# Performance work log

Hardware: AMD Instinct MI355X
Metric: run time of the kernel (lower is better)

The kernel has to match this reference:

```python
import jax, jax.numpy as jnp
import numpy as np

EPS_BN = 1e-5
EPS_NORM = 1e-12


def setup_inputs() -> dict:
    dim, mid, k = 128, 32, 3
    b, h, w = 8, 128, 128
    key = jax.random.key(0)
    ks = jax.random.split(key, 16)
    s = 0.05
    return {
        "x": jax.random.normal(ks[0], (b, dim, h, w), jnp.float32),
        "w_spatial_in": jax.random.normal(ks[1], (dim, dim), jnp.float32) * s,
        "w_dw_spatial": jax.random.normal(ks[2], (dim, 1, k), jnp.float32) * s,
        "w_spatial_out": jax.random.normal(ks[3], (dim, dim), jnp.float32) * s,
        "w_ch_in": jax.random.normal(ks[4], (dim, dim), jnp.float32) * s,
        "w_ch_dw": jax.random.normal(ks[5], (dim, 1, k), jnp.float32) * s,
        "w_ch_out": jax.random.normal(ks[6], (dim, dim), jnp.float32) * s,
        "w_mlp1": jax.random.normal(ks[7], (mid, dim), jnp.float32) * s,
        "b_mlp1": jax.random.normal(ks[8], (mid,), jnp.float32) * s,
        "w_mlp2": jax.random.normal(ks[9], (dim, mid), jnp.float32) * s,
        "b_mlp2": jax.random.normal(ks[10], (dim,), jnp.float32) * s,
        "diff_weight": jnp.float32(1.0),
        "bn_gamma": jnp.ones((dim,), jnp.float32),
        "bn_beta": jnp.zeros((dim,), jnp.float32),
        "w_out_proj": jax.random.normal(ks[11], (dim, dim), jnp.float32) * s,
    }


def _dwconv1d(seq, wk):
    # seq: [b, c, L], wk: [c, 1, k] depthwise, 'same' padding
    c = seq.shape[1]
    k = wk.shape[-1]
    return jax.lax.conv_general_dilated(
        seq, wk, window_strides=(1,), padding=[(k // 2, k // 2)],
        dimension_numbers=("NCH", "OIH", "NCH"), feature_group_count=c)


def _ocs_forward(x, w_spatial_in, w_dw_spatial, w_spatial_out,
                 w_ch_in, w_ch_dw, w_ch_out,
                 w_mlp1, b_mlp1, w_mlp2, b_mlp2,
                 diff_weight, bn_gamma, bn_beta, w_out_proj):
    b, c, h, w = x.shape
    L = h * w
    alpha = beta = eta = 1.0

    # ---- scan indices (4 orders) ----
    idx_row = jnp.arange(L)
    gy, gx = jnp.meshgrid(jnp.arange(h), jnp.arange(w), indexing="ij")
    idx_col = (gx * h + gy).reshape(-1)
    orders = [idx_row, idx_row[::-1], idx_col, idx_col[::-1]]

    x_seq0 = x.reshape(b, c, L).transpose(0, 2, 1)  # [b, L, c]

    def scan(idx):
        s = x_seq0[:, idx]                                   # gather   [b,L,c]
        s = jnp.einsum("blc,oc->blo", s, w_spatial_in)       # linear
        s = _dwconv1d(s.transpose(0, 2, 1), w_dw_spatial)    # dw conv  [b,c,L]
        s = jnp.einsum("bcl,oc->blo", s, w_spatial_out)      # linear   [b,L,c]
        s = s.at[:, idx].set(s[:, jnp.arange(L)]) if False else s[:, jnp.argsort(idx)]  # scatter back (inverse perm)
        return s.transpose(0, 2, 1).reshape(b, c, h, w)

    y_sp = (scan(orders[0]) + scan(orders[1]) + scan(orders[2]) + scan(orders[3])) * 0.25

    # ---- channel branch ----
    seq = x.reshape(b, c, L)
    seq = jnp.einsum("oc,bcl->bol", w_ch_in, seq)
    seq = _dwconv1d(seq, w_ch_dw)
    seq = jnp.einsum("oc,bcl->bol", w_ch_out, seq)
    gap = x.mean((2, 3))                                     # [b,c]
    gap = gap / jnp.maximum(jnp.linalg.norm(gap, axis=1, keepdims=True), EPS_NORM)
    m = jnp.einsum("bi,bj->bij", gap, gap)                   # [b,c,c]
    seq_agg = jnp.einsum("bij,bjl->bil", m, seq)             # [b,c,L]
    h1 = jax.nn.silu(jnp.einsum("mc,bcl->bml", w_mlp1, seq_agg) + b_mlp1[None, :, None])
    y_ch = (jnp.einsum("cm,bml->bcl", w_mlp2, h1) + b_mlp2[None, :, None]).reshape(b, c, h, w)

    # ---- difference branch (reflect-pad 4-neighbor abs diff) ----
    p = jnp.pad(x, ((0, 0), (0, 0), (1, 1), (1, 1)), mode="reflect")
    cx = p[:, :, 1:-1, 1:-1]
    diff = (jnp.abs(cx - p[:, :, 1:-1, :-2]) + jnp.abs(cx - p[:, :, 1:-1, 2:])
            + jnp.abs(cx - p[:, :, :-2, 1:-1]) + jnp.abs(cx - p[:, :, 2:, 1:-1])) * 0.25
    y_diff = x + diff_weight * diff

    # ---- combine, 1x1 proj, batchnorm (training-mode batch stats) ----
    y = alpha * y_sp + beta * y_ch + eta * y_diff
    y = jnp.einsum("oc,bchw->bohw", w_out_proj, y)
    mu = y.mean((0, 2, 3))
    var = y.var((0, 2, 3))
    y = (y - mu[None, :, None, None]) * jax.lax.rsqrt(var + EPS_BN)[None, :, None, None]
    y = y * bn_gamma[None, :, None, None] + bn_beta[None, :, None, None]
    return y


def reference(x, w_spatial_in, w_dw_spatial, w_spatial_out, w_ch_in, w_ch_dw,
              w_ch_out, w_mlp1, b_mlp1, w_mlp2, b_mlp2, diff_weight,
              bn_gamma, bn_beta, w_out_proj):
    return _ocs_forward(x, w_spatial_in, w_dw_spatial, w_spatial_out,
                        w_ch_in, w_ch_dw, w_ch_out, w_mlp1, b_mlp1,
                        w_mlp2, b_mlp2, diff_weight, bn_gamma, bn_beta,
                        w_out_proj)
```

## Files before the change

kernel.cpp:

```cpp
#include <hip/hip_runtime.h>
#include <hip/hip_bf16.h>

#define C 128
#define L 16384
#define B 8
#define MID 32
#define NBL (B * L)

typedef unsigned short ushort_t;
typedef __attribute__((ext_vector_type(8))) short s8v;
typedef __attribute__((ext_vector_type(4))) float f4v;
typedef __attribute__((ext_vector_type(8))) float f8v;

__device__ __forceinline__ unsigned short f2bf(float f) {
    union { float f; unsigned int u; } a; a.f = f;
    unsigned int u = a.u;
    return (unsigned short)((u + 0x7fffu + ((u >> 16) & 1u)) >> 16);
}

__device__ __forceinline__ f8v unp8(s8v v) {
    f8v f;
#pragma unroll
    for (int j = 0; j < 8; j++) f[j] = __uint_as_float(((unsigned int)(unsigned short)v[j]) << 16);
    return f;
}

__device__ __forceinline__ f8v ldf8(const float* p) {
    float4 a = *(const float4*)p;
    float4 b = *(const float4*)(p + 4);
    f8v f;
    f[0] = a.x; f[1] = a.y; f[2] = a.z; f[3] = a.w;
    f[4] = b.x; f[5] = b.y; f[6] = b.z; f[7] = b.w;
    return f;
}

__device__ __forceinline__ int widx(int slot, int o, int w) {
    return ((slot * 8 + (o >> 4)) * 64 + (w >> 3) * 16 + (o & 15)) * 8 + (w & 7);
}

__global__ __launch_bounds__(256) void k_cvt(const float* __restrict__ x,
                                             ushort_t* __restrict__ xb,
                                             float* __restrict__ gap) {
    __shared__ float xs[64][129];
    const int bid = blockIdx.x;
    const int b = bid >> 8;
    const int l0 = (bid & 255) * 64;
    const int tid = threadIdx.x;
    const int c = tid >> 1, h = tid & 1;
    const float* src = x + ((size_t)(b * C + c)) * L + l0 + h * 32;
    float s = 0.f;
#pragma unroll
    for (int j = 0; j < 8; j++) {
        float4 v = *(const float4*)(src + j * 4);
        s += (v.x + v.y) + (v.z + v.w);
        int lb = h * 32 + j * 4;
        xs[lb + 0][c] = v.x; xs[lb + 1][c] = v.y;
        xs[lb + 2][c] = v.z; xs[lb + 3][c] = v.w;
    }
    s += __shfl_xor(s, 1);
    if (h == 0) atomicAdd(&gap[b * C + c], s);
    __syncthreads();
    const int l = tid & 63, quarter = tid >> 6, cb = quarter * 32;
    union { ushort_t hh[32]; uint4 q[4]; } u;
#pragma unroll
    for (int k = 0; k < 32; k++) u.hh[k] = f2bf(xs[l][cb + k]);
    uint4* dst = (uint4*)(xb + ((size_t)(b * L + l0 + l)) * C + cb);
#pragma unroll
    for (int k = 0; k < 4; k++) dst[k] = u.q[k];
}

__global__ __launch_bounds__(128) void k_prep_b(const float* __restrict__ gap,
                                                const float* __restrict__ w1,
                                                const float* __restrict__ Wco,
                                                const float* __restrict__ wcd,
                                                const float* __restrict__ Wci,
                                                float* __restrict__ a,
                                                float* __restrict__ pv) {
    int b = blockIdx.x, c = threadIdx.x;
    __shared__ float gl[C];
    __shared__ float red[C];
    __shared__ float gws[C];
    float v = gap[b * C + c] * (1.f / (float)L);
    red[c] = v * v;
    __syncthreads();
    for (int w = 64; w > 0; w >>= 1) {
        if (c < w) red[c] += red[c + w];
        __syncthreads();
    }
    float nrm = fmaxf(sqrtf(red[0]), 1e-12f);
    gl[c] = v / nrm;
    __syncthreads();
    if (c < MID) {
        float s = 0.f;
        for (int k = 0; k < C; k++) s = fmaf(w1[c * C + k], gl[k], s);
        a[b * MID + c] = s;
    }
    {
        float s = 0.f;
        for (int k = 0; k < C; k++) s = fmaf(gl[k], Wco[k * C + c], s);
        gws[c] = s;
    }
    __syncthreads();
    float p0 = 0.f, p1 = 0.f, p2 = 0.f;
    for (int cc = 0; cc < C; cc++) {
        float wv = Wci[cc * C + c];
        float g = gws[cc];
        p0 = fmaf(g * wcd[3 * cc], wv, p0);
        p1 = fmaf(g * wcd[3 * cc + 1], wv, p1);
        p2 = fmaf(g * wcd[3 * cc + 2], wv, p2);
    }
    pv[b * 384 + c] = p0;
    pv[b * 384 + 128 + c] = p1;
    pv[b * 384 + 256 + c] = p2;
}

__global__ __launch_bounds__(128) void k_prep_w(const float* __restrict__ Win,
                                                const float* __restrict__ Wproj,
                                                const float* __restrict__ Wout,
                                                const float* __restrict__ w2,
                                                const float* __restrict__ b2,
                                                const float* __restrict__ wds,
                                                ushort_t* __restrict__ Wf,
                                                float* __restrict__ bp) {
    int o = blockIdx.x, c = threadIdx.x;
    __shared__ float pr[C];
    __shared__ float wct[C];
    pr[c] = Wproj[o * C + c];
    __syncthreads();
    {
        float s = 0.f;
        for (int k = 0; k < C; k++) s = fmaf(pr[k], Wout[k * C + c], s);
        wct[c] = s;
    }
    __syncthreads();
    float a1 = 0.f, as = 0.f;
    for (int cc = 0; cc < C; cc++) {
        float w = wct[cc];
        float win = Win[cc * C + c];
        a1 = fmaf(w * wds[3 * cc + 1], win, a1);
        as = fmaf(w * (0.25f * (wds[3 * cc] + wds[3 * cc + 2])), win, as);
    }
    const int slot = c >> 5, wi = c & 31;
    Wf[widx(slot, o, wi)] = f2bf(a1);
    Wf[widx(4 + slot, o, wi)] = f2bf(as);
    Wf[widx(8 + slot, o, wi)] = f2bf(pr[c]);
    if (c < MID) {
        float s2 = 0.f;
        for (int k = 0; k < C; k++) s2 = fmaf(pr[k], w2[k * MID + c], s2);
        Wf[widx(12, o, c)] = f2bf(s2);
    }
    if (c == 0) {
        float s3 = 0.f;
        for (int k = 0; k < C; k++) s3 = fmaf(pr[k], b2[k], s3);
        bp[o] = s3;
    }
}

__global__ __launch_bounds__(1024) __attribute__((amdgpu_waves_per_eu(4, 4)))
void k_fused(const ushort_t* __restrict__ xb,
             const ushort_t* __restrict__ Wf,
             const float* __restrict__ pv,
             const float* __restrict__ a,
             const float* __restrict__ b1,
             const float* __restrict__ pdw,
             const float* __restrict__ bp,
             float* __restrict__ outp,
             float* __restrict__ stats) {
    __shared__ ushort_t wlf[53248];
    __shared__ float sdst[C];
    __shared__ float sdsq[C];
    const int tid = threadIdx.x;
    int bid = blockIdx.x;
    bid = (bid & 7) * 64 + (bid >> 3);
    const int b = bid >> 6;
    const int y0 = (bid & 63) << 1;

#pragma unroll
    for (int i = 0; i < 7; i++) {
        int idx = tid + i * 1024;
        if (idx < 6656) ((uint4*)wlf)[idx] = ((const uint4*)Wf)[idx];
    }
    if (tid < C) { sdst[tid] = 0.f; sdsq[tid] = 0.f; }

    const int wave = tid >> 6, lane = tid & 63;
    const int n = lane & 15, q = lane >> 4;
    const int y = y0 + (wave >> 3);
    const int xg = (wave & 7) * 16 + n;
    const int l = y * 128 + xg;
    const size_t rb = (size_t)b * L;

    const int rL = (l > 0) ? (l - 1) : -1;
    const int rR = (l < L - 1) ? (l + 1) : -1;
    const int rU = (y > 0) ? (l - 128) : ((xg > 0) ? (16256 + xg - 1) : -1);
    const int rD = (y < 127) ? (l + 128) : ((xg < 127) ? (xg + 1) : -1);
    const int rlc = (rL >= 0) ? rL : 0;
    const int rrc = (rR >= 0) ? rR : 0;
    const int ruc = (rU >= 0) ? rU : 0;
    const int rdc = (rD >= 0) ? rD : 0;

    const float dwt4 = pdw[0] * 0.25f;
    const ushort_t* xrow = xb + (rb + l) * C;

    f4v acc[8];
#pragma unroll
    for (int i = 0; i < 8; i++) acc[i] = (f4v){0.f, 0.f, 0.f, 0.f};
    float s1 = 0.f;

    __syncthreads();

#define AF(slot, mt) (*(const s8v*)(wlf + ((((slot) * 8 + (mt)) * 64 + lane) * 8)))

#pragma unroll
    for (int ks = 0; ks < 4; ks++) {
        const int c0 = ks * 32 + q * 8;
        s8v vc = *(const s8v*)(xrow + c0);
        s8v vl = *(const s8v*)(xb + (rb + rlc) * C + c0);
        s8v vr = *(const s8v*)(xb + (rb + rrc) * C + c0);
        s8v vu = *(const s8v*)(xb + (rb + ruc) * C + c0);
        s8v vd = *(const s8v*)(xb + (rb + rdc) * C + c0);
        if (rL < 0) vl = (s8v){0, 0, 0, 0, 0, 0, 0, 0};
        if (rR < 0) vr = (s8v){0, 0, 0, 0, 0, 0, 0, 0};
        if (rU < 0) vu = (s8v){0, 0, 0, 0, 0, 0, 0, 0};
        if (rD < 0) vd = (s8v){0, 0, 0, 0, 0, 0, 0, 0};

#pragma unroll
        for (int mt = 0; mt < 8; mt++)
            acc[mt] = __builtin_amdgcn_mfma_f32_16x16x32_bf16(AF(ks, mt), vc, acc[mt], 0, 0, 0);
#pragma unroll
        for (int mt = 0; mt < 8; mt++) {
            s8v af = AF(4 + ks, mt);
            acc[mt] = __builtin_amdgcn_mfma_f32_16x16x32_bf16(af, vl, acc[mt], 0, 0, 0);
            acc[mt] = __builtin_amdgcn_mfma_f32_16x16x32_bf16(af, vr, acc[mt], 0, 0, 0);
            acc[mt] = __builtin_amdgcn_mfma_f32_16x16x32_bf16(af, vu, acc[mt], 0, 0, 0);
            acc[mt] = __builtin_amdgcn_mfma_f32_16x16x32_bf16(af, vd, acc[mt], 0, 0, 0);
        }

        f8v xc = unp8(vc);
        f8v xl = unp8(vl);
        f8v xr = unp8(vr);
        {
            f8v p0 = ldf8(pv + b * 384 + c0);
            f8v p1 = ldf8(pv + b * 384 + 128 + c0);
            f8v p2 = ldf8(pv + b * 384 + 256 + c0);
#pragma unroll
            for (int j = 0; j < 8; j++) {
                s1 = fmaf(p1[j], xc[j], s1);
                s1 = fmaf(p0[j], xl[j], s1);
                s1 = fmaf(p2[j], xr[j], s1);
            }
        }

        f8v xu = unp8(vu);
        f8v xd = unp8(vd);
        f8v a1 = (xg > 0) ? xl : xr;
        f8v a2 = (xg < 127) ? xr : xl;
        f8v a3 = (y > 0) ? xu : xd;
        f8v a4 = (y < 127) ? xd : xu;
        s8v vy;
#pragma unroll
        for (int j = 0; j < 8; j++) {
            float d = fabsf(xc[j] - a1[j]) + fabsf(xc[j] - a2[j]) +
                      fabsf(xc[j] - a3[j]) + fabsf(xc[j] - a4[j]);
            vy[j] = (short)f2bf(fmaf(dwt4, d, xc[j]));
        }
#pragma unroll
        for (int mt = 0; mt < 8; mt++)
            acc[mt] = __builtin_amdgcn_mfma_f32_16x16x32_bf16(AF(8 + ks, mt), vy, acc[mt], 0, 0, 0);
    }

    s1 += __shfl_xor(s1, 16);
    s1 += __shfl_xor(s1, 32);
    {
        f8v av = ldf8(a + b * MID + q * 8);
        f8v bv = ldf8(b1 + q * 8);
        s8v fs;
#pragma unroll
        for (int j = 0; j < 8; j++) {
            float pre = fmaf(av[j], s1, bv[j]);
            fs[j] = (short)f2bf(pre / (1.f + __expf(-pre)));
        }
#pragma unroll
        for (int mt = 0; mt < 8; mt++)
            acc[mt] = __builtin_amdgcn_mfma_f32_16x16x32_bf16(AF(12, mt), fs, acc[mt], 0, 0, 0);
    }

#undef AF

#pragma unroll
    for (int mt = 0; mt < 8; mt++) {
        const int o0 = mt * 16 + q * 4;
        float4 bv4 = *(const float4*)(bp + o0);
#pragma unroll
        for (int i = 0; i < 4; i++) {
            float bai = (i == 0) ? bv4.x : (i == 1) ? bv4.y : (i == 2) ? bv4.z : bv4.w;
            float v = acc[mt][i] + bai;
            outp[((size_t)(b * C + o0 + i)) * L + l] = v;
            float s = v, sq = v * v;
            s += __shfl_xor(s, 1); sq += __shfl_xor(sq, 1);
            s += __shfl_xor(s, 2); sq += __shfl_xor(sq, 2);
            s += __shfl_xor(s, 4); sq += __shfl_xor(sq, 4);
            s += __shfl_xor(s, 8); sq += __shfl_xor(sq, 8);
            if (n == 0) {
                atomicAdd(&sdst[o0 + i], s);
                atomicAdd(&sdsq[o0 + i], sq);
            }
        }
    }
    __syncthreads();
    if (tid < C) {
        atomicAdd(&stats[tid], sdst[tid]);
        atomicAdd(&stats[C + tid], sdsq[tid]);
    }
}

__global__ void k_bnfin(const float* __restrict__ stats, const float* __restrict__ gamma,
                        const float* __restrict__ beta, float* __restrict__ scsh) {
    int o = threadIdx.x;
    float n = (float)NBL;
    float mu = stats[o] / n;
    float var = stats[C + o] / n - mu * mu;
    float sc = gamma[o] * rsqrtf(var + 1e-5f);
    scsh[o] = sc;
    scsh[C + o] = fmaf(-mu, sc, beta[o]);
}

__global__ __launch_bounds__(256) void k_bnapply(float* __restrict__ outp,
                                                 const float* __restrict__ scsh) {
    int bo = blockIdx.x;
    int o = bo & (C - 1);
    float sc = scsh[o], sh = scsh[C + o];
    float4* p = (float4*)(outp + (size_t)bo * L);
    for (int i = threadIdx.x; i < L / 4; i += 256) {
        float4 v = p[i];
        v.x = fmaf(v.x, sc, sh);
        v.y = fmaf(v.y, sc, sh);
        v.z = fmaf(v.z, sc, sh);
        v.w = fmaf(v.w, sc, sh);
        p[i] = v;
    }
}

extern "C" void kernel_launch(void* const* d_in, const int* in_sizes, int n_in,
                              void* d_out, int out_size, void* d_ws, size_t ws_size,
                              hipStream_t stream) {
    const float* x = (const float*)d_in[0];
    const float* Win = (const float*)d_in[1];
    const float* wds = (const float*)d_in[2];
    const float* Wout = (const float*)d_in[3];
    const float* Wci = (const float*)d_in[4];
    const float* wcd = (const float*)d_in[5];
    const float* Wco = (const float*)d_in[6];
    const float* w1 = (const float*)d_in[7];
    const float* b1 = (const float*)d_in[8];
    const float* w2 = (const float*)d_in[9];
    const float* b2 = (const float*)d_in[10];
    const float* pdw = (const float*)d_in[11];
    const float* gamma = (const float*)d_in[12];
    const float* beta = (const float*)d_in[13];
    const float* Wproj = (const float*)d_in[14];

    char* wsb = (char*)d_ws;
    ushort_t* xb = (ushort_t*)wsb;
    ushort_t* Wf = (ushort_t*)(wsb + 33554432);
    char* S = wsb + 176160768;
    float* gap  = (float*)(S + 0);
    float* stats= (float*)(S + 4096);
    float* scsh = (float*)(S + 5120);
    float* a    = (float*)(S + 6144);
    float* bp   = (float*)(S + 8192);
    float* pv   = (float*)(S + 12288);
    float* outp = (float*)d_out;

    hipMemsetAsync(S, 0, 5120, stream);
    k_cvt<<<2048, 256, 0, stream>>>(x, xb, gap);
    k_prep_b<<<8, 128, 0, stream>>>(gap, w1, Wco, wcd, Wci, a, pv);
    k_prep_w<<<128, 128, 0, stream>>>(Win, Wproj, Wout, w2, b2, wds, Wf, bp);
    k_fused<<<512, 1024, 0, stream>>>(xb, Wf, pv, a, b1, pdw, bp, outp, stats);
    k_bnfin<<<1, 128, 0, stream>>>(stats, gamma, beta, scsh);
    k_bnapply<<<1024, 256, 0, stream>>>(outp, scsh);
}
```

Before: 291.7 us.

## Merge prep kernels, fold BN finalize into apply, loop fused kernel over rows

Merges the two weight/batch prep kernels into one launch and folds the BN finalize step into the apply kernel, removing two kernel launches. The fused kernel now runs 256 blocks that each loop over two row pairs, so the 104KB weight tile is staged into LDS half as often. The per-batch pv vector is also cached in shared memory, and the channel-MLP term is computed before the main MFMA loop. Fewer blocks means less parallelism and a longer serial loop per block.

```diff
diff --git a/kernel.cpp b/kernel.cpp
--- a/kernel.cpp
+++ b/kernel.cpp
@@ -69,90 +69,93 @@
     for (int k = 0; k < 4; k++) dst[k] = u.q[k];
 }
 
-__global__ __launch_bounds__(128) void k_prep_b(const float* __restrict__ gap,
-                                                const float* __restrict__ w1,
-                                                const float* __restrict__ Wco,
-                                                const float* __restrict__ wcd,
-                                                const float* __restrict__ Wci,
-                                                float* __restrict__ a,
-                                                float* __restrict__ pv) {
-    int b = blockIdx.x, c = threadIdx.x;
-    __shared__ float gl[C];
-    __shared__ float red[C];
-    __shared__ float gws[C];
-    float v = gap[b * C + c] * (1.f / (float)L);
-    red[c] = v * v;
-    __syncthreads();
-    for (int w = 64; w > 0; w >>= 1) {
-        if (c < w) red[c] += red[c + w];
+__global__ __launch_bounds__(128) void k_prep(const float* __restrict__ Win,
+                                              const float* __restrict__ Wproj,
+                                              const float* __restrict__ Wout,
+                                              const float* __restrict__ w2,
+                                              const float* __restrict__ b2,
+                                              const float* __restrict__ wds,
+                                              const float* __restrict__ gap,
+                                              const float* __restrict__ w1,
+                                              const float* __restrict__ Wco,
+                                              const float* __restrict__ wcd,
+                                              const float* __restrict__ Wci,
+                                              ushort_t* __restrict__ Wf,
+                                              float* __restrict__ bp,
+                                              float* __restrict__ a,
+                                              float* __restrict__ pv) {
+    const int bid = blockIdx.x;
+    const int c = threadIdx.x;
+    if (bid < 128) {
+        const int o = bid;
+        __shared__ float pr[C];
+        __shared__ float wct[C];
+        pr[c] = Wproj[o * C + c];
         __syncthreads();
-    }
-    float nrm = fmaxf(sqrtf(red[0]), 1e-12f);
-    gl[c] = v / nrm;
-    __syncthreads();
-    if (c < MID) {
-        float s = 0.f;
-        for (int k = 0; k < C; k++) s = fmaf(w1[c * C + k], gl[k], s);
-        a[b * MID + c] = s;
-    }
-    {
-        float s = 0.f;
-        for (int k = 0; k < C; k++) s = fmaf(gl[k], Wco[k * C + c], s);
-        gws[c] = s;
-    }
-    __syncthreads();
-    float p0 = 0.f, p1 = 0.f, p2 = 0.f;
-    for (int cc = 0; cc < C; cc++) {
-        float wv = Wci[cc * C + c];
-        float g = gws[cc];
-        p0 = fmaf(g * wcd[3 * cc], wv, p0);
-        p1 = fmaf(g * wcd[3 * cc + 1], wv, p1);
-        p2 = fmaf(g * wcd[3 * cc + 2], wv, p2);
-    }
-    pv[b * 384 + c] = p0;
-    pv[b * 384 + 128 + c] = p1;
-    pv[b * 384 + 256 + c] = p2;
-}
-
-__global__ __launch_bounds__(128) void k_prep_w(const float* __restrict__ Win,
-                                                const float* __restrict__ Wproj,
-                                                const float* __restrict__ Wout,
-                                                const float* __restrict__ w2,
-                                                const float* __restrict__ b2,
-                                                const float* __restrict__ wds,
-                                                ushort_t* __restrict__ Wf,
-                                                float* __restrict__ bp) {
-    int o = blockIdx.x, c = threadIdx.x;
-    __shared__ float pr[C];
-    __shared__ float wct[C];
-    pr[c] = Wproj[o * C + c];
-    __syncthreads();
-    {
-        float s = 0.f;
-        for (int k = 0; k < C; k++) s = fmaf(pr[k], Wout[k * C + c], s);
-        wct[c] = s;
-    }
-    __syncthreads();
-    float a1 = 0.f, as = 0.f;
-    for (int cc = 0; cc < C; cc++) {
-        float w = wct[cc];
-        float win = Win[cc * C + c];
-        a1 = fmaf(w * wds[3 * cc + 1], win, a1);
-        as = fmaf(w * (0.25f * (wds[3 * cc] + wds[3 * cc + 2])), win, as);
-    }
-    const int slot = c >> 5, wi = c & 31;
-    Wf[widx(slot, o, wi)] = f2bf(a1);
-    Wf[widx(4 + slot, o, wi)] = f2bf(as);
-    Wf[widx(8 + slot, o, wi)] = f2bf(pr[c]);
-    if (c < MID) {
-        float s2 = 0.f;
-        for (int k = 0; k < C; k++) s2 = fmaf(pr[k], w2[k * MID + c], s2);
-        Wf[widx(12, o, c)] = f2bf(s2);
-    }
-    if (c == 0) {
-        float s3 = 0.f;
-        for (int k = 0; k < C; k++) s3 = fmaf(pr[k], b2[k], s3);
-        bp[o] = s3;
+        {
+            float s = 0.f;
+            for (int k = 0; k < C; k++) s = fmaf(pr[k], Wout[k * C + c], s);
+            wct[c] = s;
+        }
+        __syncthreads();
+        float a1 = 0.f, as = 0.f;
+        for (int cc = 0; cc < C; cc++) {
+            float w = wct[cc];
+            float win = Win[cc * C + c];
+            a1 = fmaf(w * wds[3 * cc + 1], win, a1);
+            as = fmaf(w * (0.25f * (wds[3 * cc] + wds[3 * cc + 2])), win, as);
+        }
+        const int slot = c >> 5, wi = c & 31;
+        Wf[widx(slot, o, wi)] = f2bf(a1);
+        Wf[widx(4 + slot, o, wi)] = f2bf(as);
+        Wf[widx(8 + slot, o, wi)] = f2bf(pr[c]);
+        if (c < MID) {
+            float s2 = 0.f;
+            for (int k = 0; k < C; k++) s2 = fmaf(pr[k], w2[k * MID + c], s2);
+            Wf[widx(12, o, c)] = f2bf(s2);
+        }
+        if (c == 0) {
+            float s3 = 0.f;
+            for (int k = 0; k < C; k++) s3 = fmaf(pr[k], b2[k], s3);
+            bp[o] = s3;
+        }
+    } else {
+        const int b = bid - 128;
+        __shared__ float gl[C];
+        __shared__ float red[C];
+        __shared__ float gws[C];
+        float v = gap[b * C + c] * (1.f / (float)L);
+        red[c] = v * v;
+        __syncthreads();
+        for (int w = 64; w > 0; w >>= 1) {
+            if (c < w) red[c] += red[c + w];
+            __syncthreads();
+        }
+        float nrm = fmaxf(sqrtf(red[0]), 1e-12f);
+        gl[c] = v / nrm;
+        __syncthreads();
+        if (c < MID) {
+            float s = 0.f;
+            for (int k = 0; k < C; k++) s = fmaf(w1[c * C + k], gl[k], s);
+            a[b * MID + c] = s;
+        }
+        {
+            float s = 0.f;
+            for (int k = 0; k < C; k++) s = fmaf(gl[k], Wco[k * C + c], s);
+            gws[c] = s;
+        }
+        __syncthreads();
+        float p0 = 0.f, p1 = 0.f, p2 = 0.f;
+        for (int cc = 0; cc < C; cc++) {
+            float wv = Wci[cc * C + c];
+            float g = gws[cc];
+            p0 = fmaf(g * wcd[3 * cc], wv, p0);
+            p1 = fmaf(g * wcd[3 * cc + 1], wv, p1);
+            p2 = fmaf(g * wcd[3 * cc + 2], wv, p2);
+        }
+        pv[b * 384 + c] = p0;
+        pv[b * 384 + 128 + c] = p1;
+        pv[b * 384 + 256 + c] = p2;
     }
 }
 
@@ -167,145 +170,178 @@
              float* __restrict__ outp,
              float* __restrict__ stats) {
     __shared__ ushort_t wlf[53248];
+    __shared__ float spv[384];
     __shared__ float sdst[C];
     __shared__ float sdsq[C];
     const int tid = threadIdx.x;
-    int bid = blockIdx.x;
-    bid = (bid & 7) * 64 + (bid >> 3);
-    const int b = bid >> 6;
-    const int y0 = (bid & 63) << 1;
+    const int bid = blockIdx.x;
+    const int b = bid & 7;
+    const int rg = bid >> 3;
 
 #pragma unroll
     for (int i = 0; i < 7; i++) {
         int idx = tid + i * 1024;
         if (idx < 6656) ((uint4*)wlf)[idx] = ((const uint4*)Wf)[idx];
     }
+    if (tid < 384) spv[tid] = pv[b * 384 + tid];
     if (tid < C) { sdst[tid] = 0.f; sdsq[tid] = 0.f; }
 
     const int wave = tid >> 6, lane = tid & 63;
     const int n = lane & 15, q = lane >> 4;
-    const int y = y0 + (wave >> 3);
     const int xg = (wave & 7) * 16 + n;
-    const int l = y * 128 + xg;
+    const float dwt4 = pdw[0] * 0.25f;
     const size_t rb = (size_t)b * L;
 
-    const int rL = (l > 0) ? (l - 1) : -1;
-    const int rR = (l < L - 1) ? (l + 1) : -1;
-    const int rU = (y > 0) ? (l - 128) : ((xg > 0) ? (16256 + xg - 1) : -1);
-    const int rD = (y < 127) ? (l + 128) : ((xg < 127) ? (xg + 1) : -1);
-    const int rlc = (rL >= 0) ? rL : 0;
-    const int rrc = (rR >= 0) ? rR : 0;
-    const int ruc = (rU >= 0) ? rU : 0;
-    const int rdc = (rD >= 0) ? rD : 0;
-
-    const float dwt4 = pdw[0] * 0.25f;
-    const ushort_t* xrow = xb + (rb + l) * C;
-
-    f4v acc[8];
-#pragma unroll
-    for (int i = 0; i < 8; i++) acc[i] = (f4v){0.f, 0.f, 0.f, 0.f};
-    float s1 = 0.f;
-
     __syncthreads();
 
 #define AF(slot, mt) (*(const s8v*)(wlf + ((((slot) * 8 + (mt)) * 64 + lane) * 8)))
 
-#pragma unroll
-    for (int ks = 0; ks < 4; ks++) {
-        const int c0 = ks * 32 + q * 8;
-        s8v vc = *(const s8v*)(xrow + c0);
-        s8v vl = *(const s8v*)(xb + (rb + rlc) * C + c0);
-        s8v vr = *(const s8v*)(xb + (rb + rrc) * C + c0);
-        s8v vu = *(const s8v*)(xb + (rb + ruc) * C + c0);
-        s8v vd = *(const s8v*)(xb + (rb + rdc) * C + c0);
-        if (rL < 0) vl = (s8v){0, 0, 0, 0, 0, 0, 0, 0};
-        if (rR < 0) vr = (s8v){0, 0, 0, 0, 0, 0, 0, 0};
-        if (rU < 0) vu = (s8v){0, 0, 0, 0, 0, 0, 0, 0};
-        if (rD < 0) vd = (s8v){0, 0, 0, 0, 0, 0, 0, 0};
-
-#pragma unroll
-        for (int mt = 0; mt < 8; mt++)
-            acc[mt] = __builtin_amdgcn_mfma_f32_16x16x32_bf16(AF(ks, mt), vc, acc[mt], 0, 0, 0);
+#pragma unroll 1
+    for (int iter = 0; iter < 2; iter++) {
+        const int y = rg * 4 + iter * 2 + (wave >> 3);
+        const int l = y * 128 + xg;
+
+        const int rL = (l > 0) ? (l - 1) : -1;
+        const int rR = (l < L - 1) ? (l + 1) : -1;
+        const int rU = (y > 0) ? (l - 128) : ((xg > 0) ? (16256 + xg - 1) : -1);
+        const int rD = (y < 127) ? (l + 128) : ((xg < 127) ? (xg + 1) : -1);
+        const ushort_t* xrow = xb + (rb + l) * C;
+        const ushort_t* prL = xb + (rb + ((rL >= 0) ? rL : 0)) * C;
+        const ushort_t* prR = xb + (rb + ((rR >= 0) ? rR : 0)) * C;
+        const ushort_t* prU = xb + (rb + ((rU >= 0) ? rU : 0)) * C;
+        const ushort_t* prD = xb + (rb + ((rD >= 0) ? rD : 0)) * C;
+
+        float s1 = 0.f;
+#pragma unroll
+        for (int ks = 0; ks < 4; ks++) {
+            const int c0 = ks * 32 + q * 8;
+            {
+                f8v xv = unp8(*(const s8v*)(xrow + c0));
+                f8v p = ldf8(spv + 128 + c0);
+#pragma unroll
+                for (int j = 0; j < 8; j++) s1 = fmaf(p[j], xv[j], s1);
+            }
+            {
+                f8v xv = unp8(*(const s8v*)(prL + c0));
+                if (rL < 0) {
+#pragma unroll
+                    for (int j = 0; j < 8; j++) xv[j] = 0.f;
+                }
+                f8v p = ldf8(spv + c0);
+#pragma unroll
+                for (int j = 0; j < 8; j++) s1 = fmaf(p[j], xv[j], s1);
+            }
+            {
+                f8v xv = unp8(*(const s8v*)(prR + c0));
+                if (rR < 0) {
+#pragma unroll
+                    for (int j = 0; j < 8; j++) xv[j] = 0.f;
+                }
+                f8v p = ldf8(spv + 256 + c0);
+#pragma unroll
+                for (int j = 0; j < 8; j++) s1 = fmaf(p[j], xv[j], s1);
+            }
+        }
+        s1 += __shfl_xor(s1, 16);
+        s1 += __shfl_xor(s1, 32);
+
+        f4v acc[8];
+#pragma unroll
+        for (int i = 0; i < 8; i++) acc[i] = (f4v){0.f, 0.f, 0.f, 0.f};
+
+        {
+            f8v av = ldf8(a + b * MID + q * 8);
+            f8v bv = ldf8(b1 + q * 8);
+            s8v fs;
+#pragma unroll
+            for (int j = 0; j < 8; j++) {
+                float pre = fmaf(av[j], s1, bv[j]);
+                fs[j] = (short)f2bf(pre / (1.f + __expf(-pre)));
+            }
+#pragma unroll
+            for (int mt = 0; mt < 8; mt++)
+                acc[mt] = __builtin_amdgcn_mfma_f32_16x16x32_bf16(AF(12, mt), fs, acc[mt], 0, 0, 0);
+        }
+
+#pragma unroll
+        for (int ks = 0; ks < 4; ks++) {
+            const int c0 = ks * 32 + q * 8;
+            s8v vc = *(const s8v*)(xrow + c0);
+            s8v vl = *(const s8v*)(prL + c0);
+            s8v vr = *(const s8v*)(prR + c0);
+            s8v vu = *(const s8v*)(prU + c0);
+            s8v vd = *(const s8v*)(prD + c0);
+            if (rL < 0) vl = (s8v){0, 0, 0, 0, 0, 0, 0, 0};
+            if (rR < 0) vr = (s8v){0, 0, 0, 0, 0, 0, 0, 0};
+            if (rU < 0) vu = (s8v){0, 0, 0, 0, 0, 0, 0, 0};
+            if (rD < 0) vd = (s8v){0, 0, 0, 0, 0, 0, 0, 0};
+
+#pragma unroll
+            for (int mt = 0; mt < 8; mt++)
+                acc[mt] = __builtin_amdgcn_mfma_f32_16x16x32_bf16(AF(ks, mt), vc, acc[mt], 0, 0, 0);
+#pragma unroll
+            for (int mt = 0; mt < 8; mt++) {
+                s8v af = AF(4 + ks, mt);
+                acc[mt] = __builtin_amdgcn_mfma_f32_16x16x32_bf16(af, vl, acc[mt], 0, 0, 0);
+                acc[mt] = __builtin_amdgcn_mfma_f32_16x16x32_bf16(af, vr, acc[mt], 0, 0, 0);
+                acc[mt] = __builtin_amdgcn_mfma_f32_16x16x32_bf16(af, vu, acc[mt], 0, 0, 0);
+                acc[mt] = __builtin_amdgcn_mfma_f32_16x16x32_bf16(af, vd, acc[mt], 0, 0, 0);
+            }
+
+            f8v xc = unp8(vc);
+            f8v d8;
+            {
+                f8v t = unp8((xg > 0) ? vl : vr);
+#pragma unroll
+                for (int j = 0; j < 8; j++) d8[j] = fabsf(xc[j] - t[j]);
+            }
+            {
+                f8v t = unp8((xg < 127) ? vr : vl);
+#pragma unroll
+                for (int j = 0; j < 8; j++) d8[j] += fabsf(xc[j] - t[j]);
+            }
+            {
+                f8v t = unp8((y > 0) ? vu : vd);
+#pragma unroll
+                for (int j = 0; j < 8; j++) d8[j] += fabsf(xc[j] - t[j]);
+            }
+            {
+                f8v t = unp8((y < 127) ? vd : vu);
+#pragma unroll
+                for (int j = 0; j < 8; j++) d8[j] += fabsf(xc[j] - t[j]);
+            }
+            s8v vy;
+#pragma unroll
+            for (int j = 0; j < 8; j++) vy[j] = (short)f2bf(fmaf(dwt4, d8[j], xc[j]));
+#pragma unroll
+            for (int mt = 0; mt < 8; mt++)
+                acc[mt] = __builtin_amdgcn_mfma_f32_16x16x32_bf16(AF(8 + ks, mt), vy, acc[mt], 0, 0, 0);
+        }
+
 #pragma unroll
         for (int mt = 0; mt < 8; mt++) {
-            s8v af = AF(4 + ks, mt);
-            acc[mt] = __builtin_amdgcn_mfma_f32_16x16x32_bf16(af, vl, acc[mt], 0, 0, 0);
-            acc[mt] = __builtin_amdgcn_mfma_f32_16x16x32_bf16(af, vr, acc[mt], 0, 0, 0);
-            acc[mt] = __builtin_amdgcn_mfma_f32_16x16x32_bf16(af, vu, acc[mt], 0, 0, 0);
-            acc[mt] = __builtin_amdgcn_mfma_f32_16x16x32_bf16(af, vd, acc[mt], 0, 0, 0);
-        }
-
-        f8v xc = unp8(vc);
-        f8v xl = unp8(vl);
-        f8v xr = unp8(vr);
-        {
-            f8v p0 = ldf8(pv + b * 384 + c0);
-            f8v p1 = ldf8(pv + b * 384 + 128 + c0);
-            f8v p2 = ldf8(pv + b * 384 + 256 + c0);
-#pragma unroll
-            for (int j = 0; j < 8; j++) {
-                s1 = fmaf(p1[j], xc[j], s1);
-                s1 = fmaf(p0[j], xl[j], s1);
-                s1 = fmaf(p2[j], xr[j], s1);
-            }
-        }
-
-        f8v xu = unp8(vu);
-        f8v xd = unp8(vd);
-        f8v a1 = (xg > 0) ? xl : xr;
-        f8v a2 = (xg < 127) ? xr : xl;
-        f8v a3 = (y > 0) ? xu : xd;
-        f8v a4 = (y < 127) ? xd : xu;
-        s8v vy;
-#pragma unroll
-        for (int j = 0; j < 8; j++) {
-            float d = fabsf(xc[j] - a1[j]) + fabsf(xc[j] - a2[j]) +
-                      fabsf(xc[j] - a3[j]) + fabsf(xc[j] - a4[j]);
-            vy[j] = (short)f2bf(fmaf(dwt4, d, xc[j]));
-        }
-#pragma unroll
-        for (int mt = 0; mt < 8; mt++)
-            acc[mt] = __builtin_amdgcn_mfma_f32_16x16x32_bf16(AF(8 + ks, mt), vy, acc[mt], 0, 0, 0);
-    }
-
-    s1 += __shfl_xor(s1, 16);
-    s1 += __shfl_xor(s1, 32);
-    {
-        f8v av = ldf8(a + b * MID + q * 8);
-        f8v bv = ldf8(b1 + q * 8);
-        s8v fs;
-#pragma unroll
-        for (int j = 0; j < 8; j++) {
-            float pre = fmaf(av[j], s1, bv[j]);
-            fs[j] = (short)f2bf(pre / (1.f + __expf(-pre)));
-        }
-#pragma unroll
-        for (int mt = 0; mt < 8; mt++)
-            acc[mt] = __builtin_amdgcn_mfma_f32_16x16x32_bf16(AF(12, mt), fs, acc[mt], 0, 0, 0);
+            const int o0 = mt * 16 + q * 4;
+            float4 bv4 = *(const float4*)(bp + o0);
+#pragma unroll
+            for (int i = 0; i < 4; i++) {
+                float bai = (i == 0) ? bv4.x : (i == 1) ? bv4.y : (i == 2) ? bv4.z : bv4.w;
+                float v = acc[mt][i] + bai;
+                outp[((size_t)(b * C + o0 + i)) * L + l] = v;
+                float s = v, sq = v * v;
+                s += __shfl_xor(s, 1); sq += __shfl_xor(sq, 1);
+                s += __shfl_xor(s, 2); sq += __shfl_xor(sq, 2);
+                s += __shfl_xor(s, 4); sq += __shfl_xor(sq, 4);
+                s += __shfl_xor(s, 8); sq += __shfl_xor(sq, 8);
+                if (n == 0) {
+                    atomicAdd(&sdst[o0 + i], s);
+                    atomicAdd(&sdsq[o0 + i], sq);
+                }
+            }
+        }
     }
 
 #undef AF
 
-#pragma unroll
-    for (int mt = 0; mt < 8; mt++) {
-        const int o0 = mt * 16 + q * 4;
-        float4 bv4 = *(const float4*)(bp + o0);
-#pragma unroll
-        for (int i = 0; i < 4; i++) {
-            float bai = (i == 0) ? bv4.x : (i == 1) ? bv4.y : (i == 2) ? bv4.z : bv4.w;
-            float v = acc[mt][i] + bai;
-            outp[((size_t)(b * C + o0 + i)) * L + l] = v;
-            float s = v, sq = v * v;
-            s += __shfl_xor(s, 1); sq += __shfl_xor(sq, 1);
-            s += __shfl_xor(s, 2); sq += __shfl_xor(sq, 2);
-            s += __shfl_xor(s, 4); sq += __shfl_xor(sq, 4);
-            s += __shfl_xor(s, 8); sq += __shfl_xor(sq, 8);
-            if (n == 0) {
-                atomicAdd(&sdst[o0 + i], s);
-                atomicAdd(&sdsq[o0 + i], sq);
-            }
-        }
-    }
     __syncthreads();
     if (tid < C) {
         atomicAdd(&stats[tid], sdst[tid]);
@@ -313,22 +349,17 @@
     }
 }
 
-__global__ void k_bnfin(const float* __restrict__ stats, const float* __restrict__ gamma,
-                        const float* __restrict__ beta, float* __restrict__ scsh) {
-    int o = threadIdx.x;
-    float n = (float)NBL;
-    float mu = stats[o] / n;
-    float var = stats[C + o] / n - mu * mu;
-    float sc = gamma[o] * rsqrtf(var + 1e-5f);
-    scsh[o] = sc;
-    scsh[C + o] = fmaf(-mu, sc, beta[o]);
-}
-
 __global__ __launch_bounds__(256) void k_bnapply(float* __restrict__ outp,
-                                                 const float* __restrict__ scsh) {
+                                                 const float* __restrict__ stats,
+                                                 const float* __restrict__ gamma,
+                                                 const float* __restrict__ beta) {
     int bo = blockIdx.x;
     int o = bo & (C - 1);
-    float sc = scsh[o], sh = scsh[C + o];
+    float nn = (float)NBL;
+    float mu = stats[o] / nn;
+    float var = stats[C + o] / nn - mu * mu;
+    float sc = gamma[o] * rsqrtf(var + 1e-5f);
+    float sh = fmaf(-mu, sc, beta[o]);
     float4* p = (float4*)(outp + (size_t)bo * L);
     for (int i = threadIdx.x; i < L / 4; i += 256) {
         float4 v = p[i];
@@ -365,7 +396,6 @@
     char* S = wsb + 176160768;
     float* gap  = (float*)(S + 0);
     float* stats= (float*)(S + 4096);
-    float* scsh = (float*)(S + 5120);
     float* a    = (float*)(S + 6144);
     float* bp   = (float*)(S + 8192);
     float* pv   = (float*)(S + 12288);
@@ -373,9 +403,8 @@
 
     hipMemsetAsync(S, 0, 5120, stream);
     k_cvt<<<2048, 256, 0, stream>>>(x, xb, gap);
-    k_prep_b<<<8, 128, 0, stream>>>(gap, w1, Wco, wcd, Wci, a, pv);
-    k_prep_w<<<128, 128, 0, stream>>>(Win, Wproj, Wout, w2, b2, wds, Wf, bp);
-    k_fused<<<512, 1024, 0, stream>>>(xb, Wf, pv, a, b1, pdw, bp, outp, stats);
-    k_bnfin<<<1, 128, 0, stream>>>(stats, gamma, beta, scsh);
-    k_bnapply<<<1024, 256, 0, stream>>>(outp, scsh);
-}
+    k_prep<<<136, 128, 0, stream>>>(Win, Wproj, Wout, w2, b2, wds,
+                                    gap, w1, Wco, wcd, Wci, Wf, bp, a, pv);
+    k_fused<<<256, 1024, 0, stream>>>(xb, Wf, pv, a, b1, pdw, bp, outp, stats);
+    k_bnapply<<<1024, 256, 0, stream>>>(outp, stats, gamma, beta);
+}
```

Measured after the change: 279.2 us. 4.3% less time.
